# Performance work log

Measured on AMD Instinct MI355X. Metric: run time of the kernel, lower is better.

## Reference

```python
import jax, jax.numpy as jnp
import numpy as np

# ---- geometry / filter constants (from source script) ----
N0, N1, N2 = 16, 200, 200
NUM_RAD, NUM_PHI = 223, 190
VOX = 2.0                      # mm, isotropic voxel size
STEP = 2.0                     # mm, ray sampling step
SCAN_R = 350.0                 # scanner radius -> rays span [-350, 350] mm
NUM_T = int(2 * SCAN_R / STEP) + 1   # 351 samples per ray
SIGMA = 4.5 / (2.35 * VOX)     # gaussian sigma in voxels
RADIUS = int(4.0 * SIGMA + 0.5)      # scipy truncate=4 convention
ORG1 = (-N1 / 2 + 0.5) * VOX
ORG2 = (-N2 / 2 + 0.5) * VOX

_phis = np.linspace(0.0, np.pi, NUM_PHI, endpoint=False, dtype=np.float32)
COS = jnp.asarray(np.cos(_phis), dtype=jnp.float32)
SIN = jnp.asarray(np.sin(_phis), dtype=jnp.float32)
RV = jnp.asarray(np.linspace(-200.0, 200.0, NUM_RAD, dtype=np.float32))
TV = jnp.asarray(np.linspace(-SCAN_R, SCAN_R, NUM_T, dtype=np.float32))
_g = np.exp(-0.5 * (np.arange(-RADIUS, RADIUS + 1) / SIGMA) ** 2)
GW = jnp.asarray((_g / _g.sum()).astype(np.float32))


def _smooth_axis(x, axis):
    pad = [(0, 0)] * x.ndim
    pad[axis] = (RADIUS, RADIUS)
    xp = jnp.pad(x, pad, mode='symmetric')
    n = x.shape[axis]
    return sum(GW[k] * jax.lax.slice_in_dim(xp, k, k + n, axis=axis)
               for k in range(2 * RADIUS + 1))


def gauss3(x):
    # separable 3D gaussian (GaussianFilterOperator)
    for ax in range(3):
        x = _smooth_axis(x, ax)
    return x


def _bilinear(img, ix, iy):
    # img [n0, n1, n2]; ix/iy [num_rad, num_t] fractional voxel coords
    i0 = jnp.floor(ix); j0 = jnp.floor(iy)
    fi = ix - i0; fj = iy - j0
    i0 = i0.astype(jnp.int32); j0 = j0.astype(jnp.int32)
    valid = ((ix >= 0) & (ix <= N1 - 1) & (iy >= 0) & (iy <= N2 - 1)).astype(img.dtype)
    i0c = jnp.clip(i0, 0, N1 - 1); i1c = jnp.clip(i0 + 1, 0, N1 - 1)
    j0c = jnp.clip(j0, 0, N2 - 1); j1c = jnp.clip(j0 + 1, 0, N2 - 1)
    v = ((1 - fi) * (1 - fj) * img[:, i0c, j0c]
         + fi * (1 - fj) * img[:, i1c, j0c]
         + (1 - fi) * fj * img[:, i0c, j1c]
         + fi * fj * img[:, i1c, j1c])          # [n0, num_rad, num_t]
    return v * valid


def project(img):
    # ParallelViewProjector2D: line integrals per slice -> [n0, num_phi, num_rad]
    def body(_, cs):
        c, s = cs
        # ray point = r * perp(phi) + t * dir(phi); perp=(-s,c), dir=(c,s)
        ix = (RV[:, None] * (-s) + TV[None, :] * c - ORG1) / VOX
        iy = (RV[:, None] * c + TV[None, :] * s - ORG2) / VOX
        return None, _bilinear(img, ix, iy).sum(-1) * STEP
    _, sino = jax.lax.scan(body, None, (COS, SIN))   # [num_phi, n0, num_rad]
    return jnp.transpose(sino, (1, 0, 2))


def fwd_model(x, mult):
    # CompositeLinearOperator((sens_mult, projector, gaussian_filter))
    return mult * project(gauss3(x))


def adjoint_model(y, mult, like):
    # exact adjoint of the linear fwd_model via vjp
    _, vjpf = jax.vjp(lambda u: fwd_model(u, mult), jnp.zeros_like(like))
    return vjpf(y)[0]


def setup_inputs() -> dict:
    key = jax.random.key(0)
    k1, k2, k3, k4 = jax.random.split(key, 4)
    x = jax.random.uniform(k1, (N0, N1, N2), dtype=jnp.float32) + 0.1
    data = jax.random.uniform(k2, (N0, NUM_PHI, NUM_RAD), dtype=jnp.float32) * 10.0
    contamination = jax.random.uniform(k3, (N0, NUM_PHI, NUM_RAD), dtype=jnp.float32) * 0.5 + 0.5
    mult = jax.random.uniform(k4, (N0, NUM_PHI, NUM_RAD), dtype=jnp.float32) * 0.5 + 0.5
    ones_sino = jnp.ones((N0, NUM_PHI, NUM_RAD), dtype=jnp.float32)
    sens_image = jnp.maximum(adjoint_model(ones_sino, mult, x), 1e-2)
    return {"x": x, "data": data, "contamination": contamination,
            "mult": mult, "sens_image": sens_image}


def reference(x, data, contamination, mult, sens_image):
    # PoissonEMModule.forward: one MLEM update
    exp = fwd_model(x, mult) + contamination
    return x * adjoint_model(data / exp, mult, x) / sens_image
```

## Files before the change

### kernel.cpp

```cpp
#include <hip/hip_runtime.h>
#include <math.h>

#define N0 16
#define N1 200
#define N2 200
#define NPIX (N1 * N2)
#define NVOX (N0 * NPIX)
#define NUM_RAD 223
#define NUM_PHI 190
#define NUM_T 351
#define NSINO (N0 * NUM_PHI * NUM_RAD)
#define PITCH16 3328
#define S16 (3328 * 210)
#define BASEOFF16 (4 * 3328 + 4 * 16)
#define BP_CHUNK 10
#define BP_NCH 19

__global__ void init_consts(float* __restrict__ cosb, float* __restrict__ sinb,
                            float* __restrict__ rvb, float* __restrict__ gwb) {
    int t = threadIdx.x;
    const double PI = 3.14159265358979311599796346854418516159;
    if (t < NUM_PHI) {
        double step = PI / 190.0;
        float phif = (float)((double)t * step);
        cosb[t] = (float)cos((double)phif);
        sinb[t] = (float)sin((double)phif);
    }
    if (t < NUM_RAD) {
        double step = 400.0 / 222.0;
        float rv = (float)(-200.0 + (double)t * step);
        if (t == NUM_RAD - 1) rv = 200.0f;
        rvb[t] = rv;
    }
    if (t == 0) {
        double sig = 4.5 / (2.35 * 2.0);
        double g[9], ssum = 0.0;
        for (int k = 0; k < 9; ++k) { double d = (double)(k - 4) / sig; g[k] = exp(-0.5 * d * d); ssum += g[k]; }
        for (int k = 0; k < 9; ++k) gwb[k] = (float)(g[k] / ssum);
    }
}

__global__ void smooth_fwd(const float* __restrict__ in, float* __restrict__ out,
                           const float* __restrict__ gwb, int n, int stride) {
    int e = blockIdx.x * 256 + threadIdx.x;
    if (e >= NVOX) return;
    int a = (e / stride) % n;
    int base = e - a * stride;
    float sum = 0.f;
#pragma unroll
    for (int k = 0; k < 9; ++k) {
        int q = a + k - 4;
        q = (q < 0) ? (-1 - q) : ((q >= n) ? (2 * n - 1 - q) : q);
        sum = __fadd_rn(sum, __fmul_rn(gwb[k], in[base + q * stride]));
    }
    out[e] = sum;
}

__global__ void smooth_fwd2_16(const float* __restrict__ in, float* __restrict__ P16,
                               float* __restrict__ PT16, const float* __restrict__ gwb) {
    int t = blockIdx.x * 256 + threadIdx.x;
    if (t >= 2 * NPIX) return;
    int oct = t & 1;
    int pix = t >> 1;
    int i1 = pix / N2;
    int i2 = pix - i1 * N2;
    int rowbase = i1 * N2;
    float v[8];
#pragma unroll
    for (int jj = 0; jj < 8; ++jj) {
        int i0 = oct * 8 + jj;
        const float* tin = in + i0 * NPIX + rowbase;
        float sum = 0.f;
#pragma unroll
        for (int k = 0; k < 9; ++k) {
            int q = i2 + k - 4;
            q = (q < 0) ? (-1 - q) : ((q >= N2) ? (2 * N2 - 1 - q) : q);
            sum = __fadd_rn(sum, __fmul_rn(gwb[k], tin[q]));
        }
        v[jj] = sum;
    }
    int po  = BASEOFF16 + i1 * PITCH16 + i2 * 16 + oct * 8;
    int pto = BASEOFF16 + i2 * PITCH16 + i1 * 16 + oct * 8;
    *(float4*)(P16 + po)      = make_float4(v[0], v[1], v[2], v[3]);
    *(float4*)(P16 + po + 4)  = make_float4(v[4], v[5], v[6], v[7]);
    *(float4*)(PT16 + pto)     = make_float4(v[0], v[1], v[2], v[3]);
    *(float4*)(PT16 + pto + 4) = make_float4(v[4], v[5], v[6], v[7]);
}

__device__ __forceinline__ float adj_u(const float* __restrict__ in, const float* __restrict__ gwb,
                                       int base, int stride, int n, int j) {
    float r = 0.f;
#pragma unroll
    for (int k = 0; k < 9; ++k) {
        int i = j - k;
        if (i >= 0 && i < n) r = __fadd_rn(r, __fmul_rn(gwb[k], in[base + i * stride]));
    }
    return r;
}

__global__ void smooth_adj(const float* __restrict__ in, float* __restrict__ out,
                           const float* __restrict__ gwb, int n, int stride) {
    int e = blockIdx.x * 256 + threadIdx.x;
    if (e >= NVOX) return;
    int a = (e / stride) % n;
    int base = e - a * stride;
    float v = adj_u(in, gwb, base, stride, n, a + 4);
    if (a < 4)      v = __fadd_rn(v, adj_u(in, gwb, base, stride, n, 3 - a));
    if (a >= n - 4) v = __fadd_rn(v, adj_u(in, gwb, base, stride, n, 2 * n + 3 - a));
    out[e] = v;
}

__global__ void smooth_adj0_final(const float* __restrict__ in, const float* __restrict__ x,
                                  const float* __restrict__ sens, const float* __restrict__ gwb,
                                  float* __restrict__ out) {
    int e = blockIdx.x * 256 + threadIdx.x;
    if (e >= NVOX) return;
    int a = e / NPIX;
    int base = e - a * NPIX;
    float v = adj_u(in, gwb, base, NPIX, N0, a + 4);
    if (a < 4)  v = __fadd_rn(v, adj_u(in, gwb, base, NPIX, N0, 3 - a));
    if (a >= 12) v = __fadd_rn(v, adj_u(in, gwb, base, NPIX, N0, 35 - a));
    out[e] = __fdiv_rn(__fmul_rn(x[e], v), sens[e]);
}

template<bool USET>
__device__ __forceinline__ void geom2(float tv, float ch, float sh, float Ah, float Bh,
                                      float& w00, float& w10, float& w01, float& w11,
                                      int& o) {
    float ix = fmaf(tv, ch, Ah);
    float iy = fmaf(tv, sh, Bh);
    bool valid = (ix >= 0.f) & (ix <= 199.f) & (iy >= 0.f) & (iy <= 199.f);
    float fx = floorf(ix), fy = floorf(iy);
    int ii = (int)fx, jj = (int)fy;
    float fi = ix - fx, fj = iy - fy;
    int rowi = USET ? jj : ii;
    int coli = USET ? ii : jj;
    o = rowi * PITCH16 + coli * 16;
    float gi = 1.f - fi, gj = 1.f - fj;
    w00 = valid ? gi * gj : 0.f;
    w10 = valid ? fi * gj : 0.f;
    w01 = valid ? gi * fj : 0.f;
    w11 = valid ? fi * fj : 0.f;
}

template<bool USET>
__device__ __forceinline__ void ray_loop(const float* __restrict__ basep,
                                         int kbeg, int kend, float ch, float sh,
                                         float Ah, float Bh, float sums[4]) {
    constexpr int O10 = USET ? 16 : PITCH16;
    constexpr int O01 = USET ? PITCH16 : 16;
    float tv = (float)(2 * kbeg - 350);
    float w00, w10, w01, w11;
    int o;
    geom2<USET>(tv, ch, sh, Ah, Bh, w00, w10, w01, w11, o);
    float4 L00 = *(const float4*)(basep + o);
    float4 L10 = *(const float4*)(basep + o + O10);
    float4 L01 = *(const float4*)(basep + o + O01);
    float4 L11 = *(const float4*)(basep + o + O10 + O01);
#pragma unroll 2
    for (int k = kbeg; k < kend; ++k) {
        tv += 2.0f;
        float nw00, nw10, nw01, nw11;
        int no;
        geom2<USET>(tv, ch, sh, Ah, Bh, nw00, nw10, nw01, nw11, no);
        float4 N00 = *(const float4*)(basep + no);
        float4 N10 = *(const float4*)(basep + no + O10);
        float4 N01 = *(const float4*)(basep + no + O01);
        float4 N11 = *(const float4*)(basep + no + O10 + O01);
        sums[0] = fmaf(w00, L00.x, sums[0]); sums[0] = fmaf(w10, L10.x, sums[0]);
        sums[0] = fmaf(w01, L01.x, sums[0]); sums[0] = fmaf(w11, L11.x, sums[0]);
        sums[1] = fmaf(w00, L00.y, sums[1]); sums[1] = fmaf(w10, L10.y, sums[1]);
        sums[1] = fmaf(w01, L01.y, sums[1]); sums[1] = fmaf(w11, L11.y, sums[1]);
        sums[2] = fmaf(w00, L00.z, sums[2]); sums[2] = fmaf(w10, L10.z, sums[2]);
        sums[2] = fmaf(w01, L01.z, sums[2]); sums[2] = fmaf(w11, L11.z, sums[2]);
        sums[3] = fmaf(w00, L00.w, sums[3]); sums[3] = fmaf(w10, L10.w, sums[3]);
        sums[3] = fmaf(w01, L01.w, sums[3]); sums[3] = fmaf(w11, L11.w, sums[3]);
        w00 = nw00; w10 = nw10; w01 = nw01; w11 = nw11;
        L00 = N00; L10 = N10; L01 = N01; L11 = N11;
        __builtin_amdgcn_sched_group_barrier(0x002, 24, 0);
        __builtin_amdgcn_sched_group_barrier(0x020, 4, 0);
        __builtin_amdgcn_sched_group_barrier(0x002, 16, 0);
    }
    sums[0] = fmaf(w00, L00.x, sums[0]); sums[0] = fmaf(w10, L10.x, sums[0]);
    sums[0] = fmaf(w01, L01.x, sums[0]); sums[0] = fmaf(w11, L11.x, sums[0]);
    sums[1] = fmaf(w00, L00.y, sums[1]); sums[1] = fmaf(w10, L10.y, sums[1]);
    sums[1] = fmaf(w01, L01.y, sums[1]); sums[1] = fmaf(w11, L11.y, sums[1]);
    sums[2] = fmaf(w00, L00.z, sums[2]); sums[2] = fmaf(w10, L10.z, sums[2]);
    sums[2] = fmaf(w01, L01.z, sums[2]); sums[2] = fmaf(w11, L11.z, sums[2]);
    sums[3] = fmaf(w00, L00.w, sums[3]); sums[3] = fmaf(w10, L10.w, sums[3]);
    sums[3] = fmaf(w01, L01.w, sums[3]); sums[3] = fmaf(w11, L11.w, sums[3]);
}

__global__ __launch_bounds__(512, 2)
void project_ratio(const float* __restrict__ P16, const float* __restrict__ PT16,
                   const float* __restrict__ data,
                   const float* __restrict__ contam, const float* __restrict__ mult,
                   const float* __restrict__ cosb, const float* __restrict__ sinb,
                   const float* __restrict__ rvb, float* __restrict__ zt) {
    int b = blockIdx.x;
    int sw = (b & 7) * 95 + (b >> 3);
    int rc  = sw / NUM_PHI;
    int phi = sw - rc * NUM_PHI;
    int tx = threadIdx.x;
    int chunk = tx & 3;
    int rr = tx >> 2;
    int r = rc * 64 + rr;
    int half = threadIdx.y;
    bool active = (r < NUM_RAD);

    __shared__ float part[4][256];

    float sums[4] = {0.f, 0.f, 0.f, 0.f};
    float c = cosb[phi], sp = sinb[phi];
    float ch = c * 0.5f, sh = sp * 0.5f;

    bool useT = fabsf(sp) > fabsf(c);
    const float* basep = (useT ? PT16 : P16) + BASEOFF16 + chunk * 4;

    if (active) {
        float rv = rvb[r];
        float A = __fmul_rn(rv, -sp);
        float B = __fmul_rn(rv, c);
        float Ah = fmaf(rv, -sh, 99.5f);
        float Bh = fmaf(rv, ch, 99.5f);

        float tlo = -350.f, thi = 350.f;
        bool empty = false;
        if (fabsf(c) > 1e-6f) {
            float a0 = (-199.f - A) / c, b0 = (199.f - A) / c;
            tlo = fmaxf(tlo, fminf(a0, b0)); thi = fminf(thi, fmaxf(a0, b0));
        } else if (fabsf(A) > 199.5f) empty = true;
        if (fabsf(sp) > 1e-6f) {
            float a0 = (-199.f - B) / sp, b0 = (199.f - B) / sp;
            tlo = fmaxf(tlo, fminf(a0, b0)); thi = fminf(thi, fmaxf(a0, b0));
        } else if (fabsf(B) > 199.5f) empty = true;

        int klo = max(0, (int)floorf((tlo + 350.f) * 0.5f) - 1);
        int khi = min(NUM_T - 1, (int)ceilf((thi + 350.f) * 0.5f) + 1);

        if (!empty && klo <= khi) {
            int kmid = (klo + khi + 1) >> 1;
            int kbeg = half ? kmid : klo;
            int kend = half ? khi : (kmid - 1);
            if (kbeg <= kend) {
                if (useT) ray_loop<true>(basep, kbeg, kend, ch, sh, Ah, Bh, sums);
                else      ray_loop<false>(basep, kbeg, kend, ch, sh, Ah, Bh, sums);
            }
        }
    }

    if (half == 1) {
#pragma unroll
        for (int s = 0; s < 4; ++s) part[s][tx] = sums[s];
    }
    __syncthreads();
    if (half == 0 && active) {
#pragma unroll
        for (int s = 0; s < 4; ++s) {
            float proj = __fmul_rn(__fadd_rn(sums[s], part[s][tx]), 2.0f);
            int sl = chunk * 4 + s;
            int idx = (sl * NUM_PHI + phi) * NUM_RAD + r;
            float ex = __fadd_rn(__fmul_rn(mult[idx], proj), contam[idx]);
            float zval = __fmul_rn(mult[idx], __fdiv_rn(data[idx], ex));
            zt[(phi * NUM_RAD + r) * N0 + sl] = zval;
        }
    }
}

__global__ __launch_bounds__(256, 2)
void backproject(const float* __restrict__ zt, const float* __restrict__ cosb,
                 const float* __restrict__ sinb, const float* __restrict__ rvb,
                 float* __restrict__ bp) {
    int pix = blockIdx.x * 256 + threadIdx.x;
    if (pix >= NPIX) return;
    int pc = blockIdx.y;
    int i1 = pix / N2;
    int i2 = pix - i1 * N2;
    float X1 = 2.f * (float)i1 - 199.f;
    float X2 = 2.f * (float)i2 - 199.f;
    float i1f = (float)i1, i2f = (float)i2;
    float acc[N0];
#pragma unroll
    for (int i0 = 0; i0 < N0; ++i0) acc[i0] = 0.f;

    int p_end = pc * BP_CHUNK + BP_CHUNK;
    for (int p = pc * BP_CHUNK; p < p_end; ++p) {
        float c = cosb[p], sp = sinb[p];
        float ch = c * 0.5f, sh = sp * 0.5f;
        float tp = c * X1 + sp * X2;
        float rp = c * X2 - sp * X1;
        int j0 = (int)floorf((rp + 200.f) * 0.555f);
        int jb = min(max(j0 - 1, 0), NUM_RAD - 4);
        float tc = (tp + 350.f) * 0.5f;
        int kc = (int)floorf(tc + 0.5f);

        float rv4[4];
#pragma unroll
        for (int dj = 0; dj < 4; ++dj) rv4[dj] = rvb[jb + dj];

        const float4* zb = (const float4*)(zt + (p * NUM_RAD + jb) * N0);
        float4 Z[4][4];
#pragma unroll
        for (int dj = 0; dj < 4; ++dj) {
            Z[dj][0] = zb[dj * 4 + 0]; Z[dj][1] = zb[dj * 4 + 1];
            Z[dj][2] = zb[dj * 4 + 2]; Z[dj][3] = zb[dj * 4 + 3];
        }
        __builtin_amdgcn_sched_group_barrier(0x020, 20, 0);
        __builtin_amdgcn_sched_group_barrier(0x002, 220, 0);

        float tvc = (float)(2 * kc - 350);
        float Qx[3], Qy[3];
#pragma unroll
        for (int dk = 0; dk < 3; ++dk) {
            float tv = tvc + (float)(2 * (dk - 1));
            Qx[dk] = fmaf(tv, ch, 99.5f);
            Qy[dk] = fmaf(tv, sh, 99.5f);
        }
        float wv[4];
#pragma unroll
        for (int dj = 0; dj < 4; ++dj) {
            float Px = rv4[dj] * (-sh);
            float Py = rv4[dj] * ch;
            float w = 0.f;
#pragma unroll
            for (int dk = 0; dk < 3; ++dk) {
                float ix = Px + Qx[dk];
                float iy = Py + Qy[dk];
                bool valid = (ix >= 0.f) & (ix <= 199.f) & (iy >= 0.f) & (iy <= 199.f);
                float wx = fmaxf(0.f, 1.f - fabsf(ix - i1f));
                float wy = fmaxf(0.f, 1.f - fabsf(iy - i2f));
                float wxm = valid ? wx : 0.f;
                w = fmaf(wxm, wy, w);
            }
            wv[dj] = w;
        }

#pragma unroll
        for (int dj = 0; dj < 4; ++dj) {
            float w = wv[dj];
            acc[0]  = fmaf(w, Z[dj][0].x, acc[0]);  acc[1]  = fmaf(w, Z[dj][0].y, acc[1]);
            acc[2]  = fmaf(w, Z[dj][0].z, acc[2]);  acc[3]  = fmaf(w, Z[dj][0].w, acc[3]);
            acc[4]  = fmaf(w, Z[dj][1].x, acc[4]);  acc[5]  = fmaf(w, Z[dj][1].y, acc[5]);
            acc[6]  = fmaf(w, Z[dj][1].z, acc[6]);  acc[7]  = fmaf(w, Z[dj][1].w, acc[7]);
            acc[8]  = fmaf(w, Z[dj][2].x, acc[8]);  acc[9]  = fmaf(w, Z[dj][2].y, acc[9]);
            acc[10] = fmaf(w, Z[dj][2].z, acc[10]); acc[11] = fmaf(w, Z[dj][2].w, acc[11]);
            acc[12] = fmaf(w, Z[dj][3].x, acc[12]); acc[13] = fmaf(w, Z[dj][3].y, acc[13]);
            acc[14] = fmaf(w, Z[dj][3].z, acc[14]); acc[15] = fmaf(w, Z[dj][3].w, acc[15]);
        }
    }
#pragma unroll
    for (int i0 = 0; i0 < N0; ++i0)
        atomicAdd(&bp[i0 * NPIX + pix], acc[i0] * 2.0f);
}

extern "C" void kernel_launch(void* const* d_in, const int* in_sizes, int n_in,
                              void* d_out, int out_size, void* d_ws, size_t ws_size,
                              hipStream_t stream) {
    const float* x      = (const float*)d_in[0];
    const float* data   = (const float*)d_in[1];
    const float* contam = (const float*)d_in[2];
    const float* mult   = (const float*)d_in[3];
    const float* sens   = (const float*)d_in[4];
    float* out = (float*)d_out;

    float* W    = (float*)d_ws;
    float* s    = W;
    float* tmp  = W + NVOX;
    float* bp2  = W + 2 * NVOX;
    float* zt   = W + 3 * NVOX;
    float* P16  = W + 3 * NVOX + NSINO;
    float* PT16 = P16 + S16;
    float* cosb = PT16 + S16;
    float* sinb = cosb + NUM_PHI;
    float* rvb  = sinb + NUM_PHI;
    float* gwb  = rvb + NUM_RAD;

    hipLaunchKernelGGL(init_consts, dim3(1), dim3(256), 0, stream, cosb, sinb, rvb, gwb);

    int nb = (NVOX + 255) / 256;
    hipLaunchKernelGGL(smooth_fwd, dim3(nb), dim3(256), 0, stream, x,   s,   gwb, N0, NPIX);
    hipLaunchKernelGGL(smooth_fwd, dim3(nb), dim3(256), 0, stream, s,   tmp, gwb, N1, N2);
    int nb2 = (2 * NPIX + 255) / 256;
    hipLaunchKernelGGL(smooth_fwd2_16, dim3(nb2), dim3(256), 0, stream, tmp, P16, PT16, gwb);

    hipLaunchKernelGGL(project_ratio, dim3(NUM_PHI * 4), dim3(256, 2), 0, stream,
                       P16, PT16, data, contam, mult, cosb, sinb, rvb, zt);

    float* bp = s;
    hipMemsetAsync(bp, 0, NVOX * sizeof(float), stream);
    int nbp = (NPIX + 255) / 256;
    hipLaunchKernelGGL(backproject, dim3(nbp, BP_NCH), dim3(256), 0, stream,
                       zt, cosb, sinb, rvb, bp);

    hipLaunchKernelGGL(smooth_adj, dim3(nb), dim3(256), 0, stream, bp,  tmp, gwb, N2, 1);
    hipLaunchKernelGGL(smooth_adj, dim3(nb), dim3(256), 0, stream, tmp, bp2, gwb, N1, N2);
    hipLaunchKernelGGL(smooth_adj0_final, dim3(nb), dim3(256), 0, stream, bp2, x, sens, gwb, out);
}
```

Before: 303.0 us.

## Split backprojection slices across lanes and replace atomics with partial buffers

Each pixel is now handled by four lanes, and each lane accumulates four of the sixteen slices. Interpolation weights are shared between the four lanes with wave shuffles, which lowers register pressure and allows higher occupancy (launch bounds raised to 6). The angle range is split into 5 chunks instead of 19. Each chunk writes plain stores into its own scratch buffer, and a new sum5 kernel adds the five partials. This removes the atomics and the memset, at the cost of an extra elementwise pass and more memory traffic.

```diff
diff --git a/kernel.cpp b/kernel.cpp
--- a/kernel.cpp
+++ b/kernel.cpp
@@ -13,8 +13,8 @@
 #define PITCH16 3328
 #define S16 (3328 * 210)
 #define BASEOFF16 (4 * 3328 + 4 * 16)
-#define BP_CHUNK 10
-#define BP_NCH 19
+#define BP_CHUNK 38
+#define BP_NCH 5
 
 __global__ void init_consts(float* __restrict__ cosb, float* __restrict__ sinb,
                             float* __restrict__ rvb, float* __restrict__ gwb) {
@@ -121,6 +121,14 @@
     if (a < 4)  v = __fadd_rn(v, adj_u(in, gwb, base, NPIX, N0, 3 - a));
     if (a >= 12) v = __fadd_rn(v, adj_u(in, gwb, base, NPIX, N0, 35 - a));
     out[e] = __fdiv_rn(__fmul_rn(x[e], v), sens[e]);
+}
+
+__global__ void sum5(const float* __restrict__ a, const float* __restrict__ b,
+                     const float* __restrict__ c, const float* __restrict__ d,
+                     const float* __restrict__ e5, float* __restrict__ o) {
+    int e = blockIdx.x * 256 + threadIdx.x;
+    if (e >= NVOX) return;
+    o[e] = __fadd_rn(__fadd_rn(__fadd_rn(a[e], b[e]), __fadd_rn(c[e], d[e])), e5[e]);
 }
 
 template<bool USET>
@@ -267,21 +275,22 @@
     }
 }
 
-__global__ __launch_bounds__(256, 2)
+__global__ __launch_bounds__(256, 6)
 void backproject(const float* __restrict__ zt, const float* __restrict__ cosb,
                  const float* __restrict__ sinb, const float* __restrict__ rvb,
-                 float* __restrict__ bp) {
-    int pix = blockIdx.x * 256 + threadIdx.x;
-    if (pix >= NPIX) return;
+                 float* __restrict__ q0, float* __restrict__ q1, float* __restrict__ q2,
+                 float* __restrict__ q3, float* __restrict__ q4) {
+    int tx = threadIdx.x;
+    int q = tx & 3;
+    int pix = blockIdx.x * 64 + (tx >> 2);
     int pc = blockIdx.y;
     int i1 = pix / N2;
     int i2 = pix - i1 * N2;
     float X1 = 2.f * (float)i1 - 199.f;
     float X2 = 2.f * (float)i2 - 199.f;
     float i1f = (float)i1, i2f = (float)i2;
-    float acc[N0];
-#pragma unroll
-    for (int i0 = 0; i0 < N0; ++i0) acc[i0] = 0.f;
+    int lb = tx & 60;
+    float acc[4] = {0.f, 0.f, 0.f, 0.f};
 
     int p_end = pc * BP_CHUNK + BP_CHUNK;
     for (int p = pc * BP_CHUNK; p < p_end; ++p) {
@@ -294,19 +303,11 @@
         float tc = (tp + 350.f) * 0.5f;
         int kc = (int)floorf(tc + 0.5f);
 
-        float rv4[4];
-#pragma unroll
-        for (int dj = 0; dj < 4; ++dj) rv4[dj] = rvb[jb + dj];
-
         const float4* zb = (const float4*)(zt + (p * NUM_RAD + jb) * N0);
-        float4 Z[4][4];
-#pragma unroll
-        for (int dj = 0; dj < 4; ++dj) {
-            Z[dj][0] = zb[dj * 4 + 0]; Z[dj][1] = zb[dj * 4 + 1];
-            Z[dj][2] = zb[dj * 4 + 2]; Z[dj][3] = zb[dj * 4 + 3];
-        }
-        __builtin_amdgcn_sched_group_barrier(0x020, 20, 0);
-        __builtin_amdgcn_sched_group_barrier(0x002, 220, 0);
+        float4 Z0 = zb[q];
+        float4 Z1 = zb[4 + q];
+        float4 Z2 = zb[8 + q];
+        float4 Z3 = zb[12 + q];
 
         float tvc = (float)(2 * kc - 350);
         float Qx[3], Qy[3];
@@ -316,41 +317,40 @@
             Qx[dk] = fmaf(tv, ch, 99.5f);
             Qy[dk] = fmaf(tv, sh, 99.5f);
         }
-        float wv[4];
-#pragma unroll
-        for (int dj = 0; dj < 4; ++dj) {
-            float Px = rv4[dj] * (-sh);
-            float Py = rv4[dj] * ch;
-            float w = 0.f;
-#pragma unroll
-            for (int dk = 0; dk < 3; ++dk) {
-                float ix = Px + Qx[dk];
-                float iy = Py + Qy[dk];
-                bool valid = (ix >= 0.f) & (ix <= 199.f) & (iy >= 0.f) & (iy <= 199.f);
-                float wx = fmaxf(0.f, 1.f - fabsf(ix - i1f));
-                float wy = fmaxf(0.f, 1.f - fabsf(iy - i2f));
-                float wxm = valid ? wx : 0.f;
-                w = fmaf(wxm, wy, w);
-            }
-            wv[dj] = w;
-        }
-
-#pragma unroll
-        for (int dj = 0; dj < 4; ++dj) {
-            float w = wv[dj];
-            acc[0]  = fmaf(w, Z[dj][0].x, acc[0]);  acc[1]  = fmaf(w, Z[dj][0].y, acc[1]);
-            acc[2]  = fmaf(w, Z[dj][0].z, acc[2]);  acc[3]  = fmaf(w, Z[dj][0].w, acc[3]);
-            acc[4]  = fmaf(w, Z[dj][1].x, acc[4]);  acc[5]  = fmaf(w, Z[dj][1].y, acc[5]);
-            acc[6]  = fmaf(w, Z[dj][1].z, acc[6]);  acc[7]  = fmaf(w, Z[dj][1].w, acc[7]);
-            acc[8]  = fmaf(w, Z[dj][2].x, acc[8]);  acc[9]  = fmaf(w, Z[dj][2].y, acc[9]);
-            acc[10] = fmaf(w, Z[dj][2].z, acc[10]); acc[11] = fmaf(w, Z[dj][2].w, acc[11]);
-            acc[12] = fmaf(w, Z[dj][3].x, acc[12]); acc[13] = fmaf(w, Z[dj][3].y, acc[13]);
-            acc[14] = fmaf(w, Z[dj][3].z, acc[14]); acc[15] = fmaf(w, Z[dj][3].w, acc[15]);
-        }
-    }
-#pragma unroll
-    for (int i0 = 0; i0 < N0; ++i0)
-        atomicAdd(&bp[i0 * NPIX + pix], acc[i0] * 2.0f);
+        float rvj = rvb[jb + q];
+        float Px = rvj * (-sh);
+        float Py = rvj * ch;
+        float w = 0.f;
+#pragma unroll
+        for (int dk = 0; dk < 3; ++dk) {
+            float ix = Px + Qx[dk];
+            float iy = Py + Qy[dk];
+            bool valid = (ix >= 0.f) & (ix <= 199.f) & (iy >= 0.f) & (iy <= 199.f);
+            float wx = fmaxf(0.f, 1.f - fabsf(ix - i1f));
+            float wy = fmaxf(0.f, 1.f - fabsf(iy - i2f));
+            float wxm = valid ? wx : 0.f;
+            w = fmaf(wxm, wy, w);
+        }
+
+        float w0 = __shfl(w, lb + 0);
+        float w1 = __shfl(w, lb + 1);
+        float w2 = __shfl(w, lb + 2);
+        float w3 = __shfl(w, lb + 3);
+
+        acc[0] = fmaf(w0, Z0.x, acc[0]); acc[1] = fmaf(w0, Z0.y, acc[1]);
+        acc[2] = fmaf(w0, Z0.z, acc[2]); acc[3] = fmaf(w0, Z0.w, acc[3]);
+        acc[0] = fmaf(w1, Z1.x, acc[0]); acc[1] = fmaf(w1, Z1.y, acc[1]);
+        acc[2] = fmaf(w1, Z1.z, acc[2]); acc[3] = fmaf(w1, Z1.w, acc[3]);
+        acc[0] = fmaf(w2, Z2.x, acc[0]); acc[1] = fmaf(w2, Z2.y, acc[1]);
+        acc[2] = fmaf(w2, Z2.z, acc[2]); acc[3] = fmaf(w2, Z2.w, acc[3]);
+        acc[0] = fmaf(w3, Z3.x, acc[0]); acc[1] = fmaf(w3, Z3.y, acc[1]);
+        acc[2] = fmaf(w3, Z3.z, acc[2]); acc[3] = fmaf(w3, Z3.w, acc[3]);
+    }
+
+    float* pp = (pc == 0) ? q0 : (pc == 1) ? q1 : (pc == 2) ? q2 : (pc == 3) ? q3 : q4;
+#pragma unroll
+    for (int i = 0; i < 4; ++i)
+        pp[(q * 4 + i) * NPIX + pix] = acc[i] * 2.0f;
 }
 
 extern "C" void kernel_launch(void* const* d_in, const int* in_sizes, int n_in,
@@ -386,13 +386,13 @@
     hipLaunchKernelGGL(project_ratio, dim3(NUM_PHI * 4), dim3(256, 2), 0, stream,
                        P16, PT16, data, contam, mult, cosb, sinb, rvb, zt);
 
-    float* bp = s;
-    hipMemsetAsync(bp, 0, NVOX * sizeof(float), stream);
-    int nbp = (NPIX + 255) / 256;
-    hipLaunchKernelGGL(backproject, dim3(nbp, BP_NCH), dim3(256), 0, stream,
-                       zt, cosb, sinb, rvb, bp);
-
-    hipLaunchKernelGGL(smooth_adj, dim3(nb), dim3(256), 0, stream, bp,  tmp, gwb, N2, 1);
-    hipLaunchKernelGGL(smooth_adj, dim3(nb), dim3(256), 0, stream, tmp, bp2, gwb, N1, N2);
-    hipLaunchKernelGGL(smooth_adj0_final, dim3(nb), dim3(256), 0, stream, bp2, x, sens, gwb, out);
-}
+    hipLaunchKernelGGL(backproject, dim3(NPIX / 64, BP_NCH), dim3(256), 0, stream,
+                       zt, cosb, sinb, rvb, s, tmp, bp2, P16, PT16);
+
+    float* bsum = zt;
+    hipLaunchKernelGGL(sum5, dim3(nb), dim3(256), 0, stream, s, tmp, bp2, P16, PT16, bsum);
+
+    hipLaunchKernelGGL(smooth_adj, dim3(nb), dim3(256), 0, stream, bsum, s,   gwb, N2, 1);
+    hipLaunchKernelGGL(smooth_adj, dim3(nb), dim3(256), 0, stream, s,    tmp, gwb, N1, N2);
+    hipLaunchKernelGGL(smooth_adj0_final, dim3(nb), dim3(256), 0, stream, tmp, x, sens, gwb, out);
+}
```

New measurement: 269.9 us. 10.9% less time.
